# Kernel optimization log

Hardware: AMD Instinct MI355X
Metric: run time of the kernel (lower is better)

The kernel has to match this reference:

```python
import jax, jax.numpy as jnp
import numpy as np

N_NODES = 50000
N_EDGES = 800000
N_GRAPHS = 512
F_IN = 128
D = 256
EPS = 1e-5
NEG_SLOPE = 0.01  # torch LeakyReLU default


def leaky_relu(x):
    return jnp.where(x >= 0, x, NEG_SLOPE * x)


def egnn_conv(x, edge_index, edge_attr, lin2_w, lin2_b, lin_w, lin_b, n_nodes):
    # message: LeakyReLU(lin(x_j + lin2(edge_attr))), aggregate: add at target i
    src, dst = edge_index[0], edge_index[1]
    ea = edge_attr @ lin2_w.T + lin2_b          # [E, in]
    msg = (x[src] + ea) @ lin_w.T + lin_b        # [E, out]
    msg = leaky_relu(msg)
    return jax.ops.segment_sum(msg, dst, num_segments=n_nodes)


def batch_norm(x, w, b):
    # training-mode BatchNorm1d: biased batch statistics over node axis
    mean = jnp.mean(x, axis=0)
    var = jnp.mean(jnp.square(x - mean), axis=0)
    return (x - mean) * jax.lax.rsqrt(var + EPS) * w + b


def setup_inputs() -> dict:
    key = jax.random.key(0)
    ks = jax.random.split(key, 8)
    inp = {
        "node_ids": jax.random.randint(ks[0], (N_NODES,), 0, 51),
        "edge_index": jax.random.randint(ks[1], (2, N_EDGES), 0, N_NODES),
        "edge_attr": jax.random.normal(ks[2], (N_EDGES, 4), dtype=jnp.float32),
        "batch": jnp.sort(jax.random.randint(ks[3], (N_NODES,), 0, N_GRAPHS)),
        "emb_table": jax.random.normal(ks[4], (51, F_IN), dtype=jnp.float32) * 0.1,
        "c1_lin2_w": jax.random.normal(ks[5], (F_IN, 4), dtype=jnp.float32) * 0.1,
        "c1_lin2_b": jnp.zeros((F_IN,), jnp.float32),
        "c1_lin_w": jax.random.normal(ks[6], (D, F_IN), dtype=jnp.float32) * (1.0 / np.sqrt(F_IN)),
        "c1_lin_b": jnp.zeros((D,), jnp.float32),
        "bn1_w": jnp.ones((D,), jnp.float32),
        "bn1_b": jnp.zeros((D,), jnp.float32),
        "c2_lin2_w": jax.random.normal(jax.random.fold_in(key, 10), (D, 4), dtype=jnp.float32) * 0.1,
        "c2_lin2_b": jnp.zeros((D,), jnp.float32),
        "c2_lin_w": jax.random.normal(ks[7], (D, D), dtype=jnp.float32) * (1.0 / np.sqrt(D)),
        "c2_lin_b": jnp.zeros((D,), jnp.float32),
        "bn2_w": jnp.ones((D,), jnp.float32),
        "bn2_b": jnp.zeros((D,), jnp.float32),
        "gate_w": jax.random.normal(jax.random.fold_in(key, 11), (1, D), dtype=jnp.float32) * 0.1,
        "gate_b": jnp.zeros((1,), jnp.float32),
    }
    return inp


def reference(node_ids, edge_index, edge_attr, batch, emb_table,
              c1_lin2_w, c1_lin2_b, c1_lin_w, c1_lin_b, bn1_w, bn1_b,
              c2_lin2_w, c2_lin2_b, c2_lin_w, c2_lin_b, bn2_w, bn2_b,
              gate_w, gate_b):
    x = emb_table[node_ids]                                   # [N, F_IN]
    x = egnn_conv(x, edge_index, edge_attr, c1_lin2_w, c1_lin2_b,
                  c1_lin_w, c1_lin_b, N_NODES)                # [N, D]
    x = leaky_relu(batch_norm(x, bn1_w, bn1_b))
    x2 = egnn_conv(x, edge_index, edge_attr, c2_lin2_w, c2_lin2_b,
                   c2_lin_w, c2_lin_b, N_NODES)               # [N, D]
    x2 = leaky_relu(batch_norm(x2, bn2_w, bn2_b))
    # AttentionalAggregation: softmax of gate over each graph segment
    gate = x2 @ gate_w.T + gate_b                             # [N, 1]
    gmax = jax.ops.segment_max(gate, batch, num_segments=N_GRAPHS)
    e = jnp.exp(gate - gmax[batch])                           # [N, 1]
    denom = jax.ops.segment_sum(e, batch, num_segments=N_GRAPHS)
    alpha = e / denom[batch]
    out = jax.ops.segment_sum(alpha * x2, batch, num_segments=N_GRAPHS)
    return out                                                # [G, D]
```

## Files before the change

### kernel.cpp

```cpp
#include <hip/hip_runtime.h>
#include <hip/hip_bf16.h>

#define NN 50000
#define NE 800000
#define NG 512

typedef __bf16 bf16_t;
typedef __bf16 bf16x8 __attribute__((ext_vector_type(8)));
typedef __bf16 bf16x4 __attribute__((ext_vector_type(4)));
typedef float f32x4 __attribute__((ext_vector_type(4)));
typedef float f32x2 __attribute__((ext_vector_type(2)));

__device__ __forceinline__ float lrelu(float v) { return v >= 0.f ? v : 0.01f * v; }

__device__ __forceinline__ f32x2 unpk2(unsigned w) {
    union { unsigned u; float f; } lo, hi;
    lo.u = w << 16;
    hi.u = w & 0xffff0000u;
    f32x2 r; r[0] = lo.f; r[1] = hi.f; return r;
}

__global__ void gme_setup(const float* __restrict__ emb,
                          const float* __restrict__ c1lw, const float* __restrict__ c1l2w,
                          const float* __restrict__ c1l2b, const float* __restrict__ c1lb,
                          const float* __restrict__ c2lw, const float* __restrict__ c2l2w,
                          const float* __restrict__ c2l2b, const float* __restrict__ c2lb,
                          float* __restrict__ TY, float* __restrict__ WC1,
                          float* __restrict__ WC2, float* __restrict__ CB2,
                          bf16_t* __restrict__ W2B) {
    int b = blockIdx.x, t = threadIdx.x;
    if (b < 51) {
        const float4* er = (const float4*)(emb + b * 128);
        const float4* zb = (const float4*)c1l2b;
        const float4* wr = (const float4*)(c1lw + t * 128);
        float s = 0.f;
        for (int k = 0; k < 32; ++k) {
            float4 e = er[k], z = zb[k], w = wr[k];
            s += (e.x + z.x) * w.x + (e.y + z.y) * w.y + (e.z + z.z) * w.z + (e.w + z.w) * w.w;
        }
        TY[b * 256 + t] = s + c1lb[t];
    } else if (b == 51) {
        const float4* wr = (const float4*)(c1lw + t * 128);
        const float4* cw = (const float4*)c1l2w;
        float4 a = make_float4(0.f, 0.f, 0.f, 0.f);
        for (int k = 0; k < 32; ++k) {
            float4 w = wr[k];
            float4 c0 = cw[k * 4 + 0], c1 = cw[k * 4 + 1], c2 = cw[k * 4 + 2], c3 = cw[k * 4 + 3];
            a.x += w.x * c0.x + w.y * c1.x + w.z * c2.x + w.w * c3.x;
            a.y += w.x * c0.y + w.y * c1.y + w.z * c2.y + w.w * c3.y;
            a.z += w.x * c0.z + w.y * c1.z + w.z * c2.z + w.w * c3.z;
            a.w += w.x * c0.w + w.y * c1.w + w.z * c2.w + w.w * c3.w;
        }
        ((float4*)WC1)[t] = a;
    } else if (b == 52) {
        const float4* wr = (const float4*)(c2lw + t * 256);
        const float4* cw = (const float4*)c2l2w;
        const float4* zb = (const float4*)c2l2b;
        float4 a = make_float4(0.f, 0.f, 0.f, 0.f);
        float ab = 0.f;
        for (int k = 0; k < 64; ++k) {
            float4 w = wr[k];
            float4 c0 = cw[k * 4 + 0], c1 = cw[k * 4 + 1], c2 = cw[k * 4 + 2], c3 = cw[k * 4 + 3];
            float4 z = zb[k];
            a.x += w.x * c0.x + w.y * c1.x + w.z * c2.x + w.w * c3.x;
            a.y += w.x * c0.y + w.y * c1.y + w.z * c2.y + w.w * c3.y;
            a.z += w.x * c0.z + w.y * c1.z + w.z * c2.z + w.w * c3.z;
            a.w += w.x * c0.w + w.y * c1.w + w.z * c2.w + w.w * c3.w;
            ab += w.x * z.x + w.y * z.y + w.z * z.z + w.w * z.w;
        }
        ((float4*)WC2)[t] = a;
        CB2[t] = ab + c2lb[t];
    } else {
        int i0 = (b - 53) * 1024;
        for (int r = 0; r < 4; ++r) {
            int i = i0 + r * 256 + t;
            W2B[i] = (bf16_t)c2lw[i];
        }
    }
}

__global__ void gme_count(const int* __restrict__ ei, int* __restrict__ cnt) {
    int e = blockIdx.x * 256 + threadIdx.x;
    if (e >= NE) return;
    atomicAdd(&cnt[ei[NE + e]], 1);
}

__global__ void gme_scan1(const int* __restrict__ CNT, int* __restrict__ LP,
                          int* __restrict__ BS) {
    __shared__ int lds[256];
    int b = blockIdx.x, t = threadIdx.x;
    int i = b * 196 + t;
    int v = (t < 196 && i < NN) ? CNT[i] : 0;
    lds[t] = v;
    __syncthreads();
    for (int off = 1; off < 256; off <<= 1) {
        int u = (t >= off) ? lds[t - off] : 0;
        __syncthreads();
        lds[t] += u;
        __syncthreads();
    }
    if (t < 196 && i < NN) LP[i] = lds[t] - v;
    if (t == 255) BS[b] = lds[255];
}

__global__ void gme_scan2(const int* __restrict__ BS, int* __restrict__ BX,
                          int* __restrict__ RS) {
    __shared__ int lds[256];
    int t = threadIdx.x;
    int v = BS[t];
    lds[t] = v;
    __syncthreads();
    for (int off = 1; off < 256; off <<= 1) {
        int u = (t >= off) ? lds[t - off] : 0;
        __syncthreads();
        lds[t] += u;
        __syncthreads();
    }
    BX[t] = lds[t] - v;
    if (t == 255) RS[NN] = lds[255];
}

__global__ void gme_scan3(const int* __restrict__ LP, const int* __restrict__ BX,
                          int* __restrict__ RS, int* __restrict__ CUR) {
    int b = blockIdx.x, t = threadIdx.x;
    if (t >= 196) return;
    int i = b * 196 + t;
    if (i >= NN) return;
    int v = BX[b] + LP[i];
    RS[i] = v;
    CUR[i] = v;
}

__global__ void gme_scatter(const int* __restrict__ ei,
                            const float4* __restrict__ eattr,
                            const int* __restrict__ node_ids,
                            int* __restrict__ CUR, int* __restrict__ SM,
                            float4* __restrict__ SattrP) {
    int e = blockIdx.x * 256 + threadIdx.x;
    if (e >= NE) return;
    int s = ei[e];
    int d = ei[NE + e];
    int nid = node_ids[s];
    int pos = atomicAdd(&CUR[d], 1);
    SM[pos] = s | (nid << 16);
    SattrP[pos] = eattr[e];
}

__global__ __launch_bounds__(256) void gme_conv0(
        const int* __restrict__ RS, const int* __restrict__ SM,
        const float4* __restrict__ SattrP, const float* __restrict__ TY,
        const float* __restrict__ Wc, float* __restrict__ agg) {
    __shared__ __align__(16) float sTY[51 * 256];
    {
        const float4* s4 = (const float4*)TY;
        float4* d4 = (float4*)sTY;
        for (int i = threadIdx.x; i < 51 * 64; i += 256) d4[i] = s4[i];
    }
    __syncthreads();
    int lane = threadIdx.x & 63;
    const float4* wc4 = (const float4*)Wc;
    int c4 = lane * 4;
    float4 w0 = wc4[c4 + 0], w1 = wc4[c4 + 1], w2 = wc4[c4 + 2], w3 = wc4[c4 + 3];
    f32x2 wA0 = {w0.x, w1.x}, wB0 = {w0.y, w1.y}, wC0 = {w0.z, w1.z}, wD0 = {w0.w, w1.w};
    f32x2 wA1 = {w2.x, w3.x}, wB1 = {w2.y, w3.y}, wC1 = {w2.z, w3.z}, wD1 = {w2.w, w3.w};
    const f32x2 zero = {0.f, 0.f};
    const float* lrow = sTY + lane * 4;
    int base = blockIdx.x * 16 + (threadIdx.x >> 6) * 4;
#pragma unroll 1
    for (int k = 0; k < 4; ++k) {
        int node = __builtin_amdgcn_readfirstlane(base + k);
        int rs = RS[node], re = RS[node + 1];
        f32x2 accP0 = zero, accP1 = zero, accA0 = zero, accA1 = zero;
        auto accum = [&](float4 a, float4 y) {
            f32x2 y0, y1;
            y0[0] = y.x; y0[1] = y.y; y1[0] = y.z; y1[1] = y.w;
            f32x2 ax = {a.x, a.x}, ay = {a.y, a.y}, az = {a.z, a.z}, aw = {a.w, a.w};
            f32x2 m0 = __builtin_elementwise_fma(ax, wA0, y0);
            f32x2 m1 = __builtin_elementwise_fma(ax, wA1, y1);
            m0 = __builtin_elementwise_fma(ay, wB0, m0);
            m1 = __builtin_elementwise_fma(ay, wB1, m1);
            m0 = __builtin_elementwise_fma(az, wC0, m0);
            m1 = __builtin_elementwise_fma(az, wC1, m1);
            m0 = __builtin_elementwise_fma(aw, wD0, m0);
            m1 = __builtin_elementwise_fma(aw, wD1, m1);
            accA0 += m0; accA1 += m1;
            accP0 += __builtin_elementwise_max(m0, zero);
            accP1 += __builtin_elementwise_max(m1, zero);
        };
        int j = rs;
        for (; j + 4 <= re; j += 4) {
            int m0_ = SM[j], m1_ = SM[j + 1], m2_ = SM[j + 2], m3_ = SM[j + 3];
            float4 a0 = SattrP[j], a1 = SattrP[j + 1], a2 = SattrP[j + 2], a3 = SattrP[j + 3];
            float4 y0 = *(const float4*)(lrow + ((m0_ >> 16) << 8));
            float4 y1 = *(const float4*)(lrow + ((m1_ >> 16) << 8));
            float4 y2 = *(const float4*)(lrow + ((m2_ >> 16) << 8));
            float4 y3 = *(const float4*)(lrow + ((m3_ >> 16) << 8));
            accum(a0, y0); accum(a1, y1); accum(a2, y2); accum(a3, y3);
        }
        for (; j < re; ++j) {
            int m = SM[j];
            accum(SattrP[j], *(const float4*)(lrow + ((m >> 16) << 8)));
        }
        const f32x2 c99 = {0.99f, 0.99f}, c01 = {0.01f, 0.01f};
        f32x2 o0 = __builtin_elementwise_fma(accP0, c99, accA0 * c01);
        f32x2 o1 = __builtin_elementwise_fma(accP1, c99, accA1 * c01);
        *((float4*)(agg + node * 256) + lane) = make_float4(o0[0], o0[1], o1[0], o1[1]);
    }
}

__global__ __launch_bounds__(256, 4) void gme_conv1(
        const int* __restrict__ RS, const int* __restrict__ SM,
        const float4* __restrict__ SattrP, const bf16_t* __restrict__ QB,
        const float* __restrict__ Wc, float* __restrict__ agg) {
    int lane = threadIdx.x & 63;
    int node = __builtin_amdgcn_readfirstlane(blockIdx.x * 4 + (threadIdx.x >> 6));
    if (node >= NN) return;
    const float4* wc4 = (const float4*)Wc;
    int c4 = lane * 4;
    float4 w0 = wc4[c4 + 0], w1 = wc4[c4 + 1], w2 = wc4[c4 + 2], w3 = wc4[c4 + 3];
    f32x2 wA0 = {w0.x, w1.x}, wB0 = {w0.y, w1.y}, wC0 = {w0.z, w1.z}, wD0 = {w0.w, w1.w};
    f32x2 wA1 = {w2.x, w3.x}, wB1 = {w2.y, w3.y}, wC1 = {w2.z, w3.z}, wD1 = {w2.w, w3.w};
    const f32x2 zero = {0.f, 0.f};
    f32x2 accP0 = zero, accP1 = zero, accA0 = zero, accA1 = zero;
    int rs = RS[node], re = RS[node + 1];
    const char* yb = (const char*)QB;
    unsigned loff = (unsigned)(lane << 3);
    auto rowld = [&](int row) -> uint2 {
        return *(const uint2*)(yb + ((unsigned)row << 9) + loff);
    };
    auto accum = [&](float4 a, uint2 r) {
        f32x2 y0 = unpk2(r.x), y1 = unpk2(r.y);
        f32x2 ax = {a.x, a.x}, ay = {a.y, a.y}, az = {a.z, a.z}, aw = {a.w, a.w};
        f32x2 m0 = __builtin_elementwise_fma(ax, wA0, y0);
        f32x2 m1 = __builtin_elementwise_fma(ax, wA1, y1);
        m0 = __builtin_elementwise_fma(ay, wB0, m0);
        m1 = __builtin_elementwise_fma(ay, wB1, m1);
        m0 = __builtin_elementwise_fma(az, wC0, m0);
        m1 = __builtin_elementwise_fma(az, wC1, m1);
        m0 = __builtin_elementwise_fma(aw, wD0, m0);
        m1 = __builtin_elementwise_fma(aw, wD1, m1);
        accA0 += m0; accA1 += m1;
        accP0 += __builtin_elementwise_max(m0, zero);
        accP1 += __builtin_elementwise_max(m1, zero);
    };
    int j = rs;
    for (; j + 12 <= re; j += 12) {
        int s[12]; float4 a[12]; uint2 r[12];
#pragma unroll
        for (int u = 0; u < 12; ++u) s[u] = SM[j + u];
#pragma unroll
        for (int u = 0; u < 12; ++u) r[u] = rowld(s[u] & 0xffff);
#pragma unroll
        for (int u = 0; u < 12; ++u) a[u] = SattrP[j + u];
#pragma unroll
        for (int u = 0; u < 12; ++u) accum(a[u], r[u]);
    }
    if (j + 8 <= re) {
        int s[8]; float4 a[8]; uint2 r[8];
#pragma unroll
        for (int u = 0; u < 8; ++u) s[u] = SM[j + u];
#pragma unroll
        for (int u = 0; u < 8; ++u) r[u] = rowld(s[u] & 0xffff);
#pragma unroll
        for (int u = 0; u < 8; ++u) a[u] = SattrP[j + u];
#pragma unroll
        for (int u = 0; u < 8; ++u) accum(a[u], r[u]);
        j += 8;
    }
    if (j + 4 <= re) {
        int s[4]; float4 a[4]; uint2 r[4];
#pragma unroll
        for (int u = 0; u < 4; ++u) s[u] = SM[j + u];
#pragma unroll
        for (int u = 0; u < 4; ++u) r[u] = rowld(s[u] & 0xffff);
#pragma unroll
        for (int u = 0; u < 4; ++u) a[u] = SattrP[j + u];
#pragma unroll
        for (int u = 0; u < 4; ++u) accum(a[u], r[u]);
        j += 4;
    }
    for (; j < re; ++j) accum(SattrP[j], rowld(SM[j] & 0xffff));
    const f32x2 c99 = {0.99f, 0.99f}, c01 = {0.01f, 0.01f};
    f32x2 o0 = __builtin_elementwise_fma(accP0, c99, accA0 * c01);
    f32x2 o1 = __builtin_elementwise_fma(accP1, c99, accA1 * c01);
    *((float4*)(agg + node * 256) + lane) = make_float4(o0[0], o0[1], o1[0], o1[1]);
}

__global__ __launch_bounds__(256) void gme_bns1(const float* __restrict__ P,
                                                float* __restrict__ PART) {
    __shared__ float ls[4][256], lq[4][256];
    int lane = threadIdx.x & 63;
    int w = threadIdx.x >> 6;
    int b = blockIdx.x;
    int r0 = b * 98;
    int r1 = r0 + 98; if (r1 > NN) r1 = NN;
    float4 s = make_float4(0, 0, 0, 0), q = make_float4(0, 0, 0, 0);
    for (int n = r0 + w; n < r1; n += 4) {
        float4 v = ((const float4*)P)[n * 64 + lane];
        s.x += v.x; s.y += v.y; s.z += v.z; s.w += v.w;
        q.x += v.x * v.x; q.y += v.y * v.y; q.z += v.z * v.z; q.w += v.w * v.w;
    }
    int c = lane * 4;
    ls[w][c] = s.x; ls[w][c + 1] = s.y; ls[w][c + 2] = s.z; ls[w][c + 3] = s.w;
    lq[w][c] = q.x; lq[w][c + 1] = q.y; lq[w][c + 2] = q.z; lq[w][c + 3] = q.w;
    __syncthreads();
    if (w == 0) {
#pragma unroll
        for (int k = 0; k < 4; ++k) {
            int cc = c + k;
            PART[b * 512 + cc] = ls[0][cc] + ls[1][cc] + ls[2][cc] + ls[3][cc];
            PART[b * 512 + 256 + cc] = lq[0][cc] + lq[1][cc] + lq[2][cc] + lq[3][cc];
        }
    }
}

__global__ __launch_bounds__(512) void gme_bns2(const float* __restrict__ PART,
                                                float* __restrict__ ST) {
    int t = threadIdx.x;
    int b = blockIdx.x;
    float acc = 0.f;
#pragma unroll
    for (int r = 0; r < 32; ++r) acc += PART[(b * 32 + r) * 512 + t];
    atomicAdd(&ST[t], acc);
}

__global__ __launch_bounds__(256) void gme_gemm(const float* __restrict__ P,
                                                const float* __restrict__ ST,
                                                const float* __restrict__ bw,
                                                const float* __restrict__ bb,
                                                const bf16_t* __restrict__ W2B,
                                                const float* __restrict__ CB2,
                                                bf16_t* __restrict__ QB) {
    __shared__ float s_sc[256], s_sh[256];
    __shared__ __align__(16) uint4 sB[8192];
    {
        int c = threadIdx.x;
        float mean = ST[c] * (1.f / NN);
        float var = ST[256 + c] * (1.f / NN) - mean * mean;
        float sc = bw[c] * rsqrtf(var + 1e-5f);
        s_sc[c] = sc;
        s_sh[c] = bb[c] - mean * sc;
        const uint4* w4 = (const uint4*)W2B;
#pragma unroll
        for (int it = 0; it < 32; ++it) {
            int i = it * 256 + c;
            int row = i >> 5, slot = i & 31;
            sB[(row << 5) | (slot ^ (row & 7))] = w4[i];
        }
    }
    __syncthreads();
    int lane = threadIdx.x & 63;
    int wave = blockIdx.x * 4 + (threadIdx.x >> 6);
    if (wave >= NN / 16) return;
    int m0 = wave * 16;
    int r = lane & 15, q = lane >> 4;
    int rx = r & 7;
    const float* arow = P + (m0 + r) * 256 + q * 8;
    bf16x8 a[8];
#pragma unroll
    for (int kt = 0; kt < 8; ++kt) {
        int k0 = kt * 32 + q * 8;
        float4 u0 = *(const float4*)(arow + kt * 32);
        float4 u1 = *(const float4*)(arow + kt * 32 + 4);
        bf16x8 f;
        f[0] = (bf16_t)lrelu(fmaf(u0.x, s_sc[k0 + 0], s_sh[k0 + 0]));
        f[1] = (bf16_t)lrelu(fmaf(u0.y, s_sc[k0 + 1], s_sh[k0 + 1]));
        f[2] = (bf16_t)lrelu(fmaf(u0.z, s_sc[k0 + 2], s_sh[k0 + 2]));
        f[3] = (bf16_t)lrelu(fmaf(u0.w, s_sc[k0 + 3], s_sh[k0 + 3]));
        f[4] = (bf16_t)lrelu(fmaf(u1.x, s_sc[k0 + 4], s_sh[k0 + 4]));
        f[5] = (bf16_t)lrelu(fmaf(u1.y, s_sc[k0 + 5], s_sh[k0 + 5]));
        f[6] = (bf16_t)lrelu(fmaf(u1.z, s_sc[k0 + 6], s_sh[k0 + 6]));
        f[7] = (bf16_t)lrelu(fmaf(u1.w, s_sc[k0 + 7], s_sh[k0 + 7]));
        a[kt] = f;
    }
#pragma unroll 1
    for (int g = 0; g < 2; ++g) {
        f32x4 acc[8];
#pragma unroll
        for (int n8 = 0; n8 < 8; ++n8) acc[n8] = (f32x4){0.f, 0.f, 0.f, 0.f};
#pragma unroll
        for (int kt = 0; kt < 8; ++kt) {
            int slot = (kt * 4 + q) ^ rx;
            bf16x8 bf[8];
#pragma unroll
            for (int n8 = 0; n8 < 8; ++n8) {
                int row = g * 128 + n8 * 16 + r;
                bf[n8] = *(const bf16x8*)&sB[(row << 5) | slot];
            }
#pragma unroll
            for (int n8 = 0; n8 < 8; ++n8) {
                acc[n8] = __builtin_amdgcn_mfma_f32_16x16x32_bf16(bf[n8], a[kt], acc[n8], 0, 0, 0);
            }
        }
#pragma unroll
        for (int n8 = 0; n8 < 8; ++n8) {
            int nt = g * 8 + n8;
            float4 cbv = ((const float4*)CB2)[nt * 4 + q];
            bf16x4 o;
            o[0] = (bf16_t)(acc[n8][0] + cbv.x);
            o[1] = (bf16_t)(acc[n8][1] + cbv.y);
            o[2] = (bf16_t)(acc[n8][2] + cbv.z);
            o[3] = (bf16_t)(acc[n8][3] + cbv.w);
            *(bf16x4*)(QB + (m0 + r) * 256 + nt * 16 + q * 4) = o;
        }
    }
}

__global__ void gme_gstart(const int* __restrict__ batch, int* __restrict__ GS) {
    int n = blockIdx.x * 256 + threadIdx.x;
    if (n >= NN) return;
    int b = batch[n];
    if (n == 0) {
        for (int g = 0; g <= b; ++g) GS[g] = 0;
    } else {
        int a = batch[n - 1];
        for (int g = a + 1; g <= b; ++g) GS[g] = n;
    }
    if (n == NN - 1) {
        for (int g = b + 1; g <= NG; ++g) GS[g] = NN;
    }
}

__global__ __launch_bounds__(256) void gme_attn(const int* __restrict__ GS,
                                                const float* __restrict__ P,
                                                const float* __restrict__ ST,
                                                const float* __restrict__ bw,
                                                const float* __restrict__ bb,
                                                const float* __restrict__ gw,
                                                const float* __restrict__ gb,
                                                float* __restrict__ out) {
    __shared__ float gl[1024];
    __shared__ float rr[8];
    int g = blockIdx.x, t = threadIdx.x;
    int lo = GS[g], hi = GS[g + 1];
    if (lo >= hi) { out[g * 256 + t] = 0.f; return; }
    int lane = t & 63, w = t >> 6;
    {
        float4 s4 = ((const float4*)ST)[lane];
        float4 q4 = ((const float4*)(ST + 256))[lane];
        float4 w4 = ((const float4*)bw)[lane];
        float4 b4 = ((const float4*)bb)[lane];
        float4 g4 = ((const float4*)gw)[lane];
        float m0 = s4.x * (1.f / NN), m1 = s4.y * (1.f / NN);
        float m2 = s4.z * (1.f / NN), m3 = s4.w * (1.f / NN);
        float sc0 = w4.x * rsqrtf(q4.x * (1.f / NN) - m0 * m0 + 1e-5f);
        float sc1 = w4.y * rsqrtf(q4.y * (1.f / NN) - m1 * m1 + 1e-5f);
        float sc2 = w4.z * rsqrtf(q4.z * (1.f / NN) - m2 * m2 + 1e-5f);
        float sc3 = w4.w * rsqrtf(q4.w * (1.f / NN) - m3 * m3 + 1e-5f);
        float sh0 = b4.x - m0 * sc0, sh1 = b4.y - m1 * sc1;
        float sh2 = b4.z - m2 * sc2, sh3 = b4.w - m3 * sc3;
        float gb0 = gb[0];
        for (int n = lo + w; n < hi; n += 4) {
            float4 p = *(const float4*)(P + n * 256 + lane * 4);
            float d = lrelu(fmaf(p.x, sc0, sh0)) * g4.x
                    + lrelu(fmaf(p.y, sc1, sh1)) * g4.y
                    + lrelu(fmaf(p.z, sc2, sh2)) * g4.z
                    + lrelu(fmaf(p.w, sc3, sh3)) * g4.w;
#pragma unroll
            for (int off = 32; off > 0; off >>= 1) d += __shfl_xor(d, off, 64);
            if (lane == 0) gl[n - lo] = d + gb0;
        }
    }
    __syncthreads();
    int cnt = hi - lo;
    float lm = -3.0e38f;
    for (int i = t; i < cnt; i += 256) lm = fmaxf(lm, gl[i]);
#pragma unroll
    for (int off = 32; off > 0; off >>= 1) lm = fmaxf(lm, __shfl_xor(lm, off, 64));
    if (lane == 0) rr[w] = lm;
    __syncthreads();
    float mx = fmaxf(fmaxf(rr[0], rr[1]), fmaxf(rr[2], rr[3]));
    float ls = 0.f;
    for (int i = t; i < cnt; i += 256) { float e = expf(gl[i] - mx); gl[i] = e; ls += e; }
#pragma unroll
    for (int off = 32; off > 0; off >>= 1) ls += __shfl_xor(ls, off, 64);
    if (lane == 0) rr[4 + w] = ls;
    __syncthreads();
    float sinv = 1.f / (rr[4] + rr[5] + rr[6] + rr[7]);
    float mean = ST[t] * (1.f / NN);
    float var = ST[256 + t] * (1.f / NN) - mean * mean;
    float sc = bw[t] * rsqrtf(var + 1e-5f);
    float sh = bb[t] - mean * sc;
    float a0 = 0.f, a1 = 0.f, a2 = 0.f, a3 = 0.f;
    int n = lo;
    for (; n + 4 <= hi; n += 4) {
        float p0 = P[n * 256 + t], p1 = P[(n + 1) * 256 + t];
        float p2 = P[(n + 2) * 256 + t], p3 = P[(n + 3) * 256 + t];
        a0 = fmaf(gl[n - lo + 0], lrelu(fmaf(p0, sc, sh)), a0);
        a1 = fmaf(gl[n - lo + 1], lrelu(fmaf(p1, sc, sh)), a1);
        a2 = fmaf(gl[n - lo + 2], lrelu(fmaf(p2, sc, sh)), a2);
        a3 = fmaf(gl[n - lo + 3], lrelu(fmaf(p3, sc, sh)), a3);
    }
    for (; n < hi; ++n) a0 = fmaf(gl[n - lo], lrelu(fmaf(P[n * 256 + t], sc, sh)), a0);
    out[g * 256 + t] = (a0 + a1 + a2 + a3) * sinv;
}

extern "C" void kernel_launch(void* const* d_in, const int* in_sizes, int n_in,
                              void* d_out, int out_size, void* d_ws, size_t ws_size,
                              hipStream_t stream) {
    const int* node_ids = (const int*)d_in[0];
    const int* edge_index = (const int*)d_in[1];
    const float4* edge_attr = (const float4*)d_in[2];
    const int* batch = (const int*)d_in[3];
    const float* emb = (const float*)d_in[4];
    const float* c1l2w = (const float*)d_in[5];
    const float* c1l2b = (const float*)d_in[6];
    const float* c1lw = (const float*)d_in[7];
    const float* c1lb = (const float*)d_in[8];
    const float* bn1w = (const float*)d_in[9];
    const float* bn1b = (const float*)d_in[10];
    const float* c2l2w = (const float*)d_in[11];
    const float* c2l2b = (const float*)d_in[12];
    const float* c2lw = (const float*)d_in[13];
    const float* c2lb = (const float*)d_in[14];
    const float* bn2w = (const float*)d_in[15];
    const float* bn2b = (const float*)d_in[16];
    const float* gate_w = (const float*)d_in[17];
    const float* gate_b = (const float*)d_in[18];

    char* ws = (char*)d_ws;
    size_t oP = 0;
    size_t oQB = oP + 51200000;
    size_t oSattrP = oQB + 25600000;
    size_t oSM = oSattrP + 12800000;
    size_t oRS = oSM + 3200000;
    size_t oCNT = oRS + 200064;
    size_t oCUR = oCNT + 200000;
    size_t oLP = oCUR + 200000;
    size_t oBS = oLP + 200000;
    size_t oBX = oBS + 1024;
    size_t oTY = oBX + 1024;
    size_t oWC1 = oTY + 52224;
    size_t oWC2 = oWC1 + 4096;
    size_t oCB2 = oWC2 + 4096;
    size_t oW2B = oCB2 + 1024;
    size_t oST = oW2B + 131072;
    size_t oGS = oST + 4096;
    size_t oPART = oGS + 2064;

    float* P = (float*)(ws + oP);
    bf16_t* QB = (bf16_t*)(ws + oQB);
    float4* SattrP = (float4*)(ws + oSattrP);
    int* SM = (int*)(ws + oSM);
    int* RS = (int*)(ws + oRS);
    int* CNT = (int*)(ws + oCNT);
    int* CUR = (int*)(ws + oCUR);
    int* LP = (int*)(ws + oLP);
    int* BS = (int*)(ws + oBS);
    int* BX = (int*)(ws + oBX);
    float* TY = (float*)(ws + oTY);
    float* WC1 = (float*)(ws + oWC1);
    float* WC2 = (float*)(ws + oWC2);
    float* CB2 = (float*)(ws + oCB2);
    bf16_t* W2B = (bf16_t*)(ws + oW2B);
    float* ST1 = (float*)(ws + oST);
    float* ST2 = ST1 + 512;
    int* GS = (int*)(ws + oGS);
    float* PART = (float*)(ws + oPART);

    hipMemsetAsync(CNT, 0, NN * sizeof(int), stream);
    hipMemsetAsync(ST1, 0, 4096, stream);

    gme_setup<<<117, 256, 0, stream>>>(emb, c1lw, c1l2w, c1l2b, c1lb,
                                       c2lw, c2l2w, c2l2b, c2lb,
                                       TY, WC1, WC2, CB2, W2B);
    gme_count<<<NE / 256, 256, 0, stream>>>(edge_index, CNT);
    gme_scan1<<<256, 256, 0, stream>>>(CNT, LP, BS);
    gme_scan2<<<1, 256, 0, stream>>>(BS, BX, RS);
    gme_scan3<<<256, 256, 0, stream>>>(LP, BX, RS, CUR);
    gme_scatter<<<NE / 256, 256, 0, stream>>>(edge_index, edge_attr, node_ids,
                                              CUR, SM, SattrP);
    gme_gstart<<<(NN + 255) / 256, 256, 0, stream>>>(batch, GS);
    gme_conv0<<<NN / 16, 256, 0, stream>>>(RS, SM, SattrP, TY, WC1, P);
    gme_bns1<<<512, 256, 0, stream>>>(P, PART);
    gme_bns2<<<16, 512, 0, stream>>>(PART, ST1);
    gme_gemm<<<(NN / 16 + 3) / 4, 256, 0, stream>>>(P, ST1, bn1w, bn1b, W2B, CB2, QB);
    gme_conv1<<<NN / 4, 256, 0, stream>>>(RS, SM, SattrP, QB, WC2, P);
    gme_bns1<<<512, 256, 0, stream>>>(P, PART);
    gme_bns2<<<16, 512, 0, stream>>>(PART, ST2);
    gme_attn<<<NG, 256, 0, stream>>>(GS, P, ST2, bn2w, bn2b, gate_w, gate_b,
                                     (float*)d_out);
}
```

Before: 410.7 us.

## Fuse BN1 partial statistics into conv0 and deepen edge-loop unrolling

conv0 now accumulates per-channel sums and sums of squares of its outputs and writes per-block partials, so the separate bns1 pass that re-read the full node feature matrix goes away. A new reduction kernel sums the 3125 block partials. The edge loop is unrolled to 8, with a zero-valued VGPR offset added to the indices so that loads are issued in batches ahead of the FMAs. The costs are a larger partial buffer that must be reduced and extra registers from the deeper unroll.

```diff
diff --git a/kernel.cpp b/kernel.cpp
--- a/kernel.cpp
+++ b/kernel.cpp
@@ -18,6 +18,12 @@
     lo.u = w << 16;
     hi.u = w & 0xffff0000u;
     f32x2 r; r[0] = lo.f; r[1] = hi.f; return r;
+}
+
+__device__ __forceinline__ int vzero() {
+    int vz;
+    asm("v_mov_b32 %0, 0" : "=v"(vz));
+    return vz;
 }
 
 __global__ void gme_setup(const float* __restrict__ emb,
@@ -149,7 +155,8 @@
 __global__ __launch_bounds__(256) void gme_conv0(
         const int* __restrict__ RS, const int* __restrict__ SM,
         const float4* __restrict__ SattrP, const float* __restrict__ TY,
-        const float* __restrict__ Wc, float* __restrict__ agg) {
+        const float* __restrict__ Wc, float* __restrict__ agg,
+        float* __restrict__ PART) {
     __shared__ __align__(16) float sTY[51 * 256];
     {
         const float4* s4 = (const float4*)TY;
@@ -158,6 +165,8 @@
     }
     __syncthreads();
     int lane = threadIdx.x & 63;
+    int w = threadIdx.x >> 6;
+    int vz = vzero();
     const float4* wc4 = (const float4*)Wc;
     int c4 = lane * 4;
     float4 w0 = wc4[c4 + 0], w1 = wc4[c4 + 1], w2 = wc4[c4 + 2], w3 = wc4[c4 + 3];
@@ -165,7 +174,8 @@
     f32x2 wA1 = {w2.x, w3.x}, wB1 = {w2.y, w3.y}, wC1 = {w2.z, w3.z}, wD1 = {w2.w, w3.w};
     const f32x2 zero = {0.f, 0.f};
     const float* lrow = sTY + lane * 4;
-    int base = blockIdx.x * 16 + (threadIdx.x >> 6) * 4;
+    int base = blockIdx.x * 16 + w * 4;
+    f32x2 ssum0 = zero, ssum1 = zero, qsum0 = zero, qsum1 = zero;
 #pragma unroll 1
     for (int k = 0; k < 4; ++k) {
         int node = __builtin_amdgcn_readfirstlane(base + k);
@@ -188,24 +198,52 @@
             accP1 += __builtin_elementwise_max(m1, zero);
         };
         int j = rs;
-        for (; j + 4 <= re; j += 4) {
-            int m0_ = SM[j], m1_ = SM[j + 1], m2_ = SM[j + 2], m3_ = SM[j + 3];
-            float4 a0 = SattrP[j], a1 = SattrP[j + 1], a2 = SattrP[j + 2], a3 = SattrP[j + 3];
-            float4 y0 = *(const float4*)(lrow + ((m0_ >> 16) << 8));
-            float4 y1 = *(const float4*)(lrow + ((m1_ >> 16) << 8));
-            float4 y2 = *(const float4*)(lrow + ((m2_ >> 16) << 8));
-            float4 y3 = *(const float4*)(lrow + ((m3_ >> 16) << 8));
-            accum(a0, y0); accum(a1, y1); accum(a2, y2); accum(a3, y3);
+        for (; j + 8 <= re; j += 8) {
+            int m[8]; float4 a[8]; float4 y[8];
+#pragma unroll
+            for (int u = 0; u < 8; ++u) m[u] = SM[j + u + vz];
+#pragma unroll
+            for (int u = 0; u < 8; ++u) a[u] = SattrP[j + u + vz];
+#pragma unroll
+            for (int u = 0; u < 8; ++u) y[u] = *(const float4*)(lrow + ((m[u] >> 16) << 8));
+#pragma unroll
+            for (int u = 0; u < 8; ++u) accum(a[u], y[u]);
+        }
+        if (j + 4 <= re) {
+            int m[4]; float4 a[4]; float4 y[4];
+#pragma unroll
+            for (int u = 0; u < 4; ++u) m[u] = SM[j + u + vz];
+#pragma unroll
+            for (int u = 0; u < 4; ++u) a[u] = SattrP[j + u + vz];
+#pragma unroll
+            for (int u = 0; u < 4; ++u) y[u] = *(const float4*)(lrow + ((m[u] >> 16) << 8));
+#pragma unroll
+            for (int u = 0; u < 4; ++u) accum(a[u], y[u]);
+            j += 4;
         }
         for (; j < re; ++j) {
-            int m = SM[j];
-            accum(SattrP[j], *(const float4*)(lrow + ((m >> 16) << 8)));
+            int m = SM[j + vz];
+            accum(SattrP[j + vz], *(const float4*)(lrow + ((m >> 16) << 8)));
         }
         const f32x2 c99 = {0.99f, 0.99f}, c01 = {0.01f, 0.01f};
         f32x2 o0 = __builtin_elementwise_fma(accP0, c99, accA0 * c01);
         f32x2 o1 = __builtin_elementwise_fma(accP1, c99, accA1 * c01);
         *((float4*)(agg + node * 256) + lane) = make_float4(o0[0], o0[1], o1[0], o1[1]);
-    }
+        ssum0 += o0; ssum1 += o1;
+        qsum0 += o0 * o0; qsum1 += o1 * o1;
+    }
+    __syncthreads();
+    float* red = sTY;
+    red[w * 512 + c4 + 0] = ssum0[0]; red[w * 512 + c4 + 1] = ssum0[1];
+    red[w * 512 + c4 + 2] = ssum1[0]; red[w * 512 + c4 + 3] = ssum1[1];
+    red[w * 512 + 256 + c4 + 0] = qsum0[0]; red[w * 512 + 256 + c4 + 1] = qsum0[1];
+    red[w * 512 + 256 + c4 + 2] = qsum1[0]; red[w * 512 + 256 + c4 + 3] = qsum1[1];
+    __syncthreads();
+    int cc = threadIdx.x;
+    float s = red[cc] + red[512 + cc] + red[1024 + cc] + red[1536 + cc];
+    float q = red[256 + cc] + red[768 + cc] + red[1280 + cc] + red[1792 + cc];
+    PART[blockIdx.x * 512 + cc] = s;
+    PART[blockIdx.x * 512 + 256 + cc] = q;
 }
 
 __global__ __launch_bounds__(256, 4) void gme_conv1(
@@ -324,6 +362,17 @@
     atomicAdd(&ST[t], acc);
 }
 
+__global__ __launch_bounds__(512) void gme_bns2a(const float* __restrict__ PART,
+                                                 float* __restrict__ ST) {
+    int t = threadIdx.x;
+    int b = blockIdx.x;
+    int r0 = b * 196;
+    int r1 = r0 + 196; if (r1 > 3125) r1 = 3125;
+    float acc = 0.f;
+    for (int r = r0; r < r1; ++r) acc += PART[r * 512 + t];
+    atomicAdd(&ST[t], acc);
+}
+
 __global__ __launch_bounds__(256) void gme_gemm(const float* __restrict__ P,
                                                 const float* __restrict__ ST,
                                                 const float* __restrict__ bw,
@@ -571,9 +620,8 @@
     gme_scatter<<<NE / 256, 256, 0, stream>>>(edge_index, edge_attr, node_ids,
                                               CUR, SM, SattrP);
     gme_gstart<<<(NN + 255) / 256, 256, 0, stream>>>(batch, GS);
-    gme_conv0<<<NN / 16, 256, 0, stream>>>(RS, SM, SattrP, TY, WC1, P);
-    gme_bns1<<<512, 256, 0, stream>>>(P, PART);
-    gme_bns2<<<16, 512, 0, stream>>>(PART, ST1);
+    gme_conv0<<<NN / 16, 256, 0, stream>>>(RS, SM, SattrP, TY, WC1, P, PART);
+    gme_bns2a<<<16, 512, 0, stream>>>(PART, ST1);
     gme_gemm<<<(NN / 16 + 3) / 4, 256, 0, stream>>>(P, ST1, bn1w, bn1b, W2B, CB2, QB);
     gme_conv1<<<NN / 4, 256, 0, stream>>>(RS, SM, SattrP, QB, WC2, P);
     gme_bns1<<<512, 256, 0, stream>>>(P, PART);
```

After: 463.2 us. 1.13x slower.
